# Optimization experiments

Measured on AMD Instinct MI355X. Metric: run time of the kernel, lower is better.

Reference implementation:

```python
import jax, jax.numpy as jnp
import numpy as np

B, IN, H = 4096, 1024, 2048


def setup_inputs() -> dict:
    key = jax.random.key(0)
    ks = jax.random.split(key, 7)
    return {
        "x": jax.random.normal(ks[0], (B, IN), jnp.float32),
        "h": jax.random.normal(ks[1], (B, H), jnp.float32),
        "c": jax.random.normal(ks[2], (B, H), jnp.float32),
        "w_ih": jax.random.normal(ks[3], (4 * H, IN), jnp.float32) * 0.02,
        "w_hh": jax.random.normal(ks[4], (4 * H, H), jnp.float32) * 0.02,
        "b_ih": jax.random.normal(ks[5], (4 * H,), jnp.float32) * 0.02,
        "b_hh": jax.random.normal(ks[6], (4 * H,), jnp.float32) * 0.02,
    }


def reference(x, h, c, w_ih, w_hh, b_ih, b_hh):
    act = jnp.sin  # custom gate activation (Sine_activation repo)
    # Combined GEMMs: same math as the 8 separate F.linear calls.
    # gates: [B, 4H], chunk order along dim 0 of weights: f, i, ic, o
    gates = (x @ w_ih.T + b_ih) + (h @ w_hh.T + b_hh)
    f_in, i_in, ic_in, o_in = jnp.split(gates, 4, axis=-1)
    ft = jax.nn.sigmoid(f_in)
    it = jax.nn.sigmoid(i_in)
    i_cands = act(ic_in)
    ct = c * ft + i_cands * it
    ot = jax.nn.sigmoid(o_in)
    ht = ot * act(ct)
    return (ht, ct)
```

## Files before the change

kernel.cpp:

```cpp
#include <hip/hip_runtime.h>

typedef __attribute__((ext_vector_type(8))) short short8;
typedef __attribute__((ext_vector_type(4))) float f32x4;

#define BDIM 4096
#define INDIM 1024
#define HDIM 2048
#define KDIM 3072
#define NDIM 8192
#define OUT_HALF 8388608
#define NKT 96

__device__ __forceinline__ unsigned short f2bf(float f) {
  unsigned u = __float_as_uint(f);
  u += 0x7FFFu + ((u >> 16) & 1u);
  return (unsigned short)(u >> 16);
}

__device__ __forceinline__ float sigmoidf_(float x) {
  return 1.0f / (1.0f + __expf(-x));
}

__global__ __launch_bounds__(256) void pack_a(const float* __restrict__ x,
                                              const float* __restrict__ hh,
                                              unsigned short* __restrict__ A) {
  int idx = blockIdx.x * 256 + threadIdx.x;
  int m = idx / 384;
  int k0 = (idx - m * 384) * 8;
  const float* src = (k0 < INDIM) ? (x + (size_t)m * INDIM + k0)
                                  : (hh + (size_t)m * HDIM + (k0 - INDIM));
  float4 lo = ((const float4*)src)[0];
  float4 hi = ((const float4*)src)[1];
  union { unsigned short us[8]; uint4 v; } o;
  o.us[0] = f2bf(lo.x); o.us[1] = f2bf(lo.y); o.us[2] = f2bf(lo.z); o.us[3] = f2bf(lo.w);
  o.us[4] = f2bf(hi.x); o.us[5] = f2bf(hi.y); o.us[6] = f2bf(hi.z); o.us[7] = f2bf(hi.w);
  *(uint4*)(A + (size_t)m * KDIM + k0) = o.v;
}

__global__ __launch_bounds__(256) void pack_w(const float* __restrict__ w_ih,
                                              const float* __restrict__ w_hh,
                                              const float* __restrict__ b_ih,
                                              const float* __restrict__ b_hh,
                                              unsigned short* __restrict__ W,
                                              float* __restrict__ bias) {
  int idx = blockIdx.x * 256 + threadIdx.x;
  int np = idx / 384;
  int rem = idx - np * 384;
  int k0 = rem * 8;
  int j = np >> 2;
  int g = np & 3;
  int n = g * HDIM + j;
  const float* src = (k0 < INDIM) ? (w_ih + (size_t)n * INDIM + k0)
                                  : (w_hh + (size_t)n * HDIM + (k0 - INDIM));
  float4 lo = ((const float4*)src)[0];
  float4 hi = ((const float4*)src)[1];
  union { unsigned short us[8]; uint4 v; } o;
  o.us[0] = f2bf(lo.x); o.us[1] = f2bf(lo.y); o.us[2] = f2bf(lo.z); o.us[3] = f2bf(lo.w);
  o.us[4] = f2bf(hi.x); o.us[5] = f2bf(hi.y); o.us[6] = f2bf(hi.z); o.us[7] = f2bf(hi.w);
  *(uint4*)(W + (size_t)np * KDIM + k0) = o.v;
  if (rem == 0) bias[np] = b_ih[n] + b_hh[n];
}

__device__ __forceinline__ void gload_lds16(const void* g, void* l) {
  __builtin_amdgcn_global_load_lds(
      (const __attribute__((address_space(1))) void*)g,
      (__attribute__((address_space(3))) void*)l, 16, 0, 0);
}

__global__ __launch_bounds__(512, 2) void lstm_gemm(
    const unsigned short* __restrict__ A,
    const unsigned short* __restrict__ W,
    const float* __restrict__ bias,
    const float* __restrict__ c,
    float* __restrict__ out) {
  extern __shared__ char smem[];

  const int tid = threadIdx.x;
  const int lane = tid & 63;
  const int wid = tid >> 6;

  const int bid = blockIdx.x;
  const int local = bid >> 3;
  const int tm = (bid & 7) * 2 + (local & 1);
  const int tn = local >> 1;

  int rowA0, clA0, rowA1, clA1, rowB0, clB0, rowB1, clB1;
  {
    int P0 = wid * 1024 + lane * 16;
    int P1 = 8192 + wid * 1024 + lane * 16;
    int r2, cp, cg;
    r2 = P0 >> 7; cp = (P0 >> 4) & 7; cg = cp ^ (r2 & 7);
    rowA0 = r2 * 2 + (cg >> 2); clA0 = cg & 3;
    r2 = P1 >> 7; cp = (P1 >> 4) & 7; cg = cp ^ (r2 & 7);
    rowA1 = r2 * 2 + (cg >> 2); clA1 = cg & 3;
    rowB0 = rowA0; clB0 = clA0;
    rowB1 = rowA1; clB1 = clA1;
  }
  const unsigned short* srcA0 = A + (size_t)(tm * 256 + rowA0) * KDIM + clA0 * 8;
  const unsigned short* srcA1 = A + (size_t)(tm * 256 + rowA1) * KDIM + clA1 * 8;
  const unsigned short* srcB0 = W + (size_t)(tn * 256 + rowB0) * KDIM + clB0 * 8;
  const unsigned short* srcB1 = W + (size_t)(tn * 256 + rowB1) * KDIM + clB1 * 8;
  const int ldA0 = wid * 1024;
  const int ldA1 = 8192 + wid * 1024;
  const int ldB0 = 16384 + wid * 1024;
  const int ldB1 = 24576 + wid * 1024;

  const int fr = lane & 15;
  const int fq = lane >> 4;
  const int wr = wid >> 2;
  const int wc = wid & 3;
  const int frh = fr >> 1;
  const int clA = (((fr & 1) << 2) | fq) ^ frh;
  const int aconst = wr * 8192 + frh * 128 + clA * 16;
  const int bconst = 16384 + wc * 4096 + frh * 128 + clA * 16;

  f32x4 acc[8][4] = {};

#pragma unroll
  for (int tt = 0; tt < 3; ++tt) {
    char* lb = smem + tt * 32768;
    gload_lds16(srcA0 + tt * 32, lb + ldA0);
    gload_lds16(srcA1 + tt * 32, lb + ldA1);
    gload_lds16(srcB0 + tt * 32, lb + ldB0);
    gload_lds16(srcB1 + tt * 32, lb + ldB1);
  }

#define TILE_BODY(T, VMSTR, STAGE_)                                          \
  do {                                                                       \
    const char* rb = smem + ((T) & 3) * 32768;                               \
    char* lb = smem + (((T) + 3) & 3) * 32768;                               \
    if (STAGE_) {                                                            \
      gload_lds16(srcA0 + (size_t)((T) + 3) * 32, lb + ldA0);                \
      gload_lds16(srcA1 + (size_t)((T) + 3) * 32, lb + ldA1);                \
    }                                                                        \
    asm volatile("s_waitcnt vmcnt(" VMSTR ")" ::: "memory");                 \
    __builtin_amdgcn_s_barrier();                                            \
    short8 bf_[4], af[4];                                                    \
    _Pragma("unroll")                                                        \
    for (int ni = 0; ni < 4; ++ni)                                           \
      bf_[ni] = *(const short8*)(rb + bconst + ni * 1024);                   \
    _Pragma("unroll")                                                        \
    for (int mi = 0; mi < 4; ++mi)                                           \
      af[mi] = *(const short8*)(rb + aconst + mi * 1024);                    \
    __builtin_amdgcn_s_setprio(1);                                           \
    _Pragma("unroll")                                                        \
    for (int mi = 0; mi < 4; ++mi)                                           \
      _Pragma("unroll")                                                      \
      for (int ni = 0; ni < 4; ++ni)                                         \
        acc[mi][ni] = __builtin_amdgcn_mfma_f32_16x16x32_bf16(               \
            af[mi], bf_[ni], acc[mi][ni], 0, 0, 0);                          \
    __builtin_amdgcn_s_setprio(0);                                           \
    if (STAGE_) {                                                            \
      gload_lds16(srcB0 + (size_t)((T) + 3) * 32, lb + ldB0);                \
      gload_lds16(srcB1 + (size_t)((T) + 3) * 32, lb + ldB1);                \
    }                                                                        \
    short8 ag[4];                                                            \
    _Pragma("unroll")                                                        \
    for (int mi = 0; mi < 4; ++mi)                                           \
      ag[mi] = *(const short8*)(rb + aconst + (mi + 4) * 1024);              \
    __builtin_amdgcn_s_setprio(1);                                           \
    _Pragma("unroll")                                                        \
    for (int mi = 0; mi < 4; ++mi)                                           \
      _Pragma("unroll")                                                      \
      for (int ni = 0; ni < 4; ++ni)                                         \
        acc[mi + 4][ni] = __builtin_amdgcn_mfma_f32_16x16x32_bf16(           \
            ag[mi], bf_[ni], acc[mi + 4][ni], 0, 0, 0);                      \
    __builtin_amdgcn_s_setprio(0);                                           \
    asm volatile("s_waitcnt lgkmcnt(0)" ::: "memory");                       \
    __builtin_amdgcn_s_barrier();                                            \
  } while (0)

  for (int t = 0; t < NKT - 3; ++t) TILE_BODY(t, "10", true);
  TILE_BODY(NKT - 3, "8", false);
  TILE_BODY(NKT - 2, "4", false);
  TILE_BODY(NKT - 1, "0", false);
#undef TILE_BODY

  const int jw = fr;
  const int jg = tn * 64 + wc * 16 + jw;
  const f32x4 bi = *(const f32x4*)(bias + tn * 256 + wc * 64 + jw * 4);
  float* ep = (float*)smem + wid * 1024;

#pragma unroll
  for (int mi = 0; mi < 8; ++mi) {
#pragma unroll
    for (int ni = 0; ni < 4; ++ni)
#pragma unroll
      for (int r = 0; r < 4; ++r)
        ep[(fq * 4 + r) * 64 + ni * 16 + fr] = acc[mi][ni][r];
    asm volatile("s_waitcnt lgkmcnt(0)" ::: "memory");
#pragma unroll
    for (int t4 = 0; t4 < 4; ++t4) {
      const int row = fq + t4 * 4;
      f32x4 g4 = *(const f32x4*)(ep + row * 64 + jw * 4);
      const float f_in = g4[0] + bi[0];
      const float i_in = g4[1] + bi[1];
      const float ic_in = g4[2] + bi[2];
      const float o_in = g4[3] + bi[3];
      const float ft = sigmoidf_(f_in);
      const float it = sigmoidf_(i_in);
      const float ics = __sinf(ic_in);
      const int mg = tm * 256 + wr * 128 + mi * 16 + row;
      const float cv = c[(size_t)mg * HDIM + jg];
      const float ct = cv * ft + ics * it;
      const float ot = sigmoidf_(o_in);
      const float ht = ot * __sinf(ct);
      out[(size_t)mg * HDIM + jg] = ht;
      out[OUT_HALF + (size_t)mg * HDIM + jg] = ct;
    }
    asm volatile("s_waitcnt lgkmcnt(0)" ::: "memory");
  }
}

extern "C" void kernel_launch(void* const* d_in, const int* in_sizes, int n_in,
                              void* d_out, int out_size, void* d_ws, size_t ws_size,
                              hipStream_t stream) {
  const float* x    = (const float*)d_in[0];
  const float* h    = (const float*)d_in[1];
  const float* c    = (const float*)d_in[2];
  const float* w_ih = (const float*)d_in[3];
  const float* w_hh = (const float*)d_in[4];
  const float* b_ih = (const float*)d_in[5];
  const float* b_hh = (const float*)d_in[6];
  float* out = (float*)d_out;

  char* ws = (char*)d_ws;
  unsigned short* Abf = (unsigned short*)ws;
  unsigned short* Wbf = (unsigned short*)(ws + 25165824);
  float* bias = (float*)(ws + 25165824 + 50331648);

  static_assert(sizeof(void*) == 8, "");
  hipFuncSetAttribute((const void*)lstm_gemm,
                      hipFuncAttributeMaxDynamicSharedMemorySize, 131072);

  pack_a<<<6144, 256, 0, stream>>>(x, h, Abf);
  pack_w<<<12288, 256, 0, stream>>>(w_ih, w_hh, b_ih, b_hh, Wbf, bias);
  lstm_gemm<<<512, 512, 131072, stream>>>(Abf, Wbf, bias, c, out);
}
```

Baseline: 233.5 us.

## Prefetch next K-tile LDS fragments into registers and merge barriers per tile

Restructures the GEMM main loop so the A and B fragments for the next K tile are read from LDS into registers while the current tile's second MFMA half runs. The two barriers per iteration become one, placed mid-tile, and sched_barrier fences pin the instruction order. The vmcnt wait thresholds are recomputed to match. This hides LDS read latency behind MFMAs at the cost of more live registers and a tighter synchronization scheme that could race if the counts are wrong.

```diff
diff --git a/kernel.cpp b/kernel.cpp
--- a/kernel.cpp
+++ b/kernel.cpp
@@ -67,6 +67,8 @@
       (__attribute__((address_space(3))) void*)l, 16, 0, 0);
 }
 
+#define SB0 __builtin_amdgcn_sched_barrier(0)
+
 __global__ __launch_bounds__(512, 2) void lstm_gemm(
     const unsigned short* __restrict__ A,
     const unsigned short* __restrict__ W,
@@ -84,7 +86,7 @@
   const int tm = (bid & 7) * 2 + (local & 1);
   const int tn = local >> 1;
 
-  int rowA0, clA0, rowA1, clA1, rowB0, clB0, rowB1, clB1;
+  int rowA0, clA0, rowA1, clA1;
   {
     int P0 = wid * 1024 + lane * 16;
     int P1 = 8192 + wid * 1024 + lane * 16;
@@ -93,13 +95,11 @@
     rowA0 = r2 * 2 + (cg >> 2); clA0 = cg & 3;
     r2 = P1 >> 7; cp = (P1 >> 4) & 7; cg = cp ^ (r2 & 7);
     rowA1 = r2 * 2 + (cg >> 2); clA1 = cg & 3;
-    rowB0 = rowA0; clB0 = clA0;
-    rowB1 = rowA1; clB1 = clA1;
   }
   const unsigned short* srcA0 = A + (size_t)(tm * 256 + rowA0) * KDIM + clA0 * 8;
   const unsigned short* srcA1 = A + (size_t)(tm * 256 + rowA1) * KDIM + clA1 * 8;
-  const unsigned short* srcB0 = W + (size_t)(tn * 256 + rowB0) * KDIM + clB0 * 8;
-  const unsigned short* srcB1 = W + (size_t)(tn * 256 + rowB1) * KDIM + clB1 * 8;
+  const unsigned short* srcB0 = W + (size_t)(tn * 256 + rowA0) * KDIM + clA0 * 8;
+  const unsigned short* srcB1 = W + (size_t)(tn * 256 + rowA1) * KDIM + clA1 * 8;
   const int ldA0 = wid * 1024;
   const int ldA1 = 8192 + wid * 1024;
   const int ldB0 = 16384 + wid * 1024;
@@ -115,6 +115,7 @@
   const int bconst = 16384 + wc * 4096 + frh * 128 + clA * 16;
 
   f32x4 acc[8][4] = {};
+  short8 af[4], bf_[4], ag[4];
 
 #pragma unroll
   for (int tt = 0; tt < 3; ++tt) {
@@ -124,24 +125,28 @@
     gload_lds16(srcB0 + tt * 32, lb + ldB0);
     gload_lds16(srcB1 + tt * 32, lb + ldB1);
   }
-
-#define TILE_BODY(T, VMSTR, STAGE_)                                          \
+  asm volatile("s_waitcnt vmcnt(8)" ::: "memory");
+  __builtin_amdgcn_s_barrier(); SB0;
+#pragma unroll
+  for (int mi = 0; mi < 4; ++mi)
+    af[mi] = *(const short8*)(smem + aconst + mi * 1024);
+#pragma unroll
+  for (int ni = 0; ni < 4; ++ni)
+    bf_[ni] = *(const short8*)(smem + bconst + ni * 1024);
+
+#define TILE_BODY(T, VMSTR, STAGE_, PREF_)                                   \
   do {                                                                       \
     const char* rb = smem + ((T) & 3) * 32768;                               \
+    const char* rbn = smem + (((T) + 1) & 3) * 32768;                        \
     char* lb = smem + (((T) + 3) & 3) * 32768;                               \
     if (STAGE_) {                                                            \
       gload_lds16(srcA0 + (size_t)((T) + 3) * 32, lb + ldA0);                \
       gload_lds16(srcA1 + (size_t)((T) + 3) * 32, lb + ldA1);                \
     }                                                                        \
-    asm volatile("s_waitcnt vmcnt(" VMSTR ")" ::: "memory");                 \
-    __builtin_amdgcn_s_barrier();                                            \
-    short8 bf_[4], af[4];                                                    \
-    _Pragma("unroll")                                                        \
-    for (int ni = 0; ni < 4; ++ni)                                           \
-      bf_[ni] = *(const short8*)(rb + bconst + ni * 1024);                   \
     _Pragma("unroll")                                                        \
     for (int mi = 0; mi < 4; ++mi)                                           \
-      af[mi] = *(const short8*)(rb + aconst + mi * 1024);                    \
+      ag[mi] = *(const short8*)(rb + aconst + (mi + 4) * 1024);              \
+    SB0;                                                                     \
     __builtin_amdgcn_s_setprio(1);                                           \
     _Pragma("unroll")                                                        \
     for (int mi = 0; mi < 4; ++mi)                                           \
@@ -154,10 +159,15 @@
       gload_lds16(srcB0 + (size_t)((T) + 3) * 32, lb + ldB0);                \
       gload_lds16(srcB1 + (size_t)((T) + 3) * 32, lb + ldB1);                \
     }                                                                        \
-    short8 ag[4];                                                            \
-    _Pragma("unroll")                                                        \
-    for (int mi = 0; mi < 4; ++mi)                                           \
-      ag[mi] = *(const short8*)(rb + aconst + (mi + 4) * 1024);              \
+    asm volatile("s_waitcnt vmcnt(" VMSTR ")" ::: "memory");                 \
+    asm volatile("s_waitcnt lgkmcnt(0)" ::: "memory");                       \
+    __builtin_amdgcn_s_barrier(); SB0;                                       \
+    if (PREF_) {                                                             \
+      _Pragma("unroll")                                                      \
+      for (int mi = 0; mi < 4; ++mi)                                         \
+        af[mi] = *(const short8*)(rbn + aconst + mi * 1024);                 \
+    }                                                                        \
+    SB0;                                                                     \
     __builtin_amdgcn_s_setprio(1);                                           \
     _Pragma("unroll")                                                        \
     for (int mi = 0; mi < 4; ++mi)                                           \
@@ -166,14 +176,17 @@
         acc[mi + 4][ni] = __builtin_amdgcn_mfma_f32_16x16x32_bf16(           \
             ag[mi], bf_[ni], acc[mi + 4][ni], 0, 0, 0);                      \
     __builtin_amdgcn_s_setprio(0);                                           \
-    asm volatile("s_waitcnt lgkmcnt(0)" ::: "memory");                       \
-    __builtin_amdgcn_s_barrier();                                            \
+    if (PREF_) {                                                             \
+      _Pragma("unroll")                                                      \
+      for (int ni = 0; ni < 4; ++ni)                                         \
+        bf_[ni] = *(const short8*)(rbn + bconst + ni * 1024);                \
+    }                                                                        \
   } while (0)
 
-  for (int t = 0; t < NKT - 3; ++t) TILE_BODY(t, "10", true);
-  TILE_BODY(NKT - 3, "8", false);
-  TILE_BODY(NKT - 2, "4", false);
-  TILE_BODY(NKT - 1, "0", false);
+  for (int t = 0; t < NKT - 3; ++t) TILE_BODY(t, "8", true, true);
+  TILE_BODY(NKT - 3, "4", false, true);
+  TILE_BODY(NKT - 2, "0", false, true);
+  TILE_BODY(NKT - 1, "0", false, false);
 #undef TILE_BODY
 
   const int jw = fr;
@@ -229,7 +242,6 @@
   unsigned short* Wbf = (unsigned short*)(ws + 25165824);
   float* bias = (float*)(ws + 25165824 + 50331648);
 
-  static_assert(sizeof(void*) == 8, "");
   hipFuncSetAttribute((const void*)lstm_gemm,
                       hipFuncAttributeMaxDynamicSharedMemorySize, 131072);
 
```

Measured after the change: 222.6 us. -4.6%, faster.

## Restructure GEMM main loop to K=64 double-buffered tiles with split staging

Applied to the files above, without the earlier changes.

The main GEMM loop moves from a 4-deep ring of K=32 tiles to two 64KB buffers of K=64 tiles, and uses a new XOR swizzle. Each tile is split into four MFMA clusters, with A and B halves staged asynchronously between clusters behind barriers, so global-to-LDS loads overlap compute with fewer full-tile syncs. The two pack kernels are merged into one launch, and the epilogue LDS row stride is padded to 68 to reduce bank conflicts. The cost is more barriers per tile and shallower prefetch depth, which may expose memory latency.

```diff
diff --git a/kernel.cpp b/kernel.cpp
--- a/kernel.cpp
+++ b/kernel.cpp
@@ -9,7 +9,8 @@
 #define KDIM 3072
 #define NDIM 8192
 #define OUT_HALF 8388608
-#define NKT 96
+#define NKT 48
+#define ACHUNKS 1572864
 
 __device__ __forceinline__ unsigned short f2bf(float f) {
   unsigned u = __float_as_uint(f);
@@ -21,44 +22,42 @@
   return 1.0f / (1.0f + __expf(-x));
 }
 
-__global__ __launch_bounds__(256) void pack_a(const float* __restrict__ x,
-                                              const float* __restrict__ hh,
-                                              unsigned short* __restrict__ A) {
+__global__ __launch_bounds__(256) void pack_all(
+    const float* __restrict__ x, const float* __restrict__ hh,
+    const float* __restrict__ w_ih, const float* __restrict__ w_hh,
+    const float* __restrict__ b_ih, const float* __restrict__ b_hh,
+    unsigned short* __restrict__ A, unsigned short* __restrict__ W,
+    float* __restrict__ bias) {
   int idx = blockIdx.x * 256 + threadIdx.x;
-  int m = idx / 384;
-  int k0 = (idx - m * 384) * 8;
-  const float* src = (k0 < INDIM) ? (x + (size_t)m * INDIM + k0)
-                                  : (hh + (size_t)m * HDIM + (k0 - INDIM));
-  float4 lo = ((const float4*)src)[0];
-  float4 hi = ((const float4*)src)[1];
-  union { unsigned short us[8]; uint4 v; } o;
-  o.us[0] = f2bf(lo.x); o.us[1] = f2bf(lo.y); o.us[2] = f2bf(lo.z); o.us[3] = f2bf(lo.w);
-  o.us[4] = f2bf(hi.x); o.us[5] = f2bf(hi.y); o.us[6] = f2bf(hi.z); o.us[7] = f2bf(hi.w);
-  *(uint4*)(A + (size_t)m * KDIM + k0) = o.v;
-}
-
-__global__ __launch_bounds__(256) void pack_w(const float* __restrict__ w_ih,
-                                              const float* __restrict__ w_hh,
-                                              const float* __restrict__ b_ih,
-                                              const float* __restrict__ b_hh,
-                                              unsigned short* __restrict__ W,
-                                              float* __restrict__ bias) {
-  int idx = blockIdx.x * 256 + threadIdx.x;
-  int np = idx / 384;
-  int rem = idx - np * 384;
-  int k0 = rem * 8;
-  int j = np >> 2;
-  int g = np & 3;
-  int n = g * HDIM + j;
-  const float* src = (k0 < INDIM) ? (w_ih + (size_t)n * INDIM + k0)
-                                  : (w_hh + (size_t)n * HDIM + (k0 - INDIM));
-  float4 lo = ((const float4*)src)[0];
-  float4 hi = ((const float4*)src)[1];
-  union { unsigned short us[8]; uint4 v; } o;
-  o.us[0] = f2bf(lo.x); o.us[1] = f2bf(lo.y); o.us[2] = f2bf(lo.z); o.us[3] = f2bf(lo.w);
-  o.us[4] = f2bf(hi.x); o.us[5] = f2bf(hi.y); o.us[6] = f2bf(hi.z); o.us[7] = f2bf(hi.w);
-  *(uint4*)(W + (size_t)np * KDIM + k0) = o.v;
-  if (rem == 0) bias[np] = b_ih[n] + b_hh[n];
+  if (idx < ACHUNKS) {
+    int m = idx / 384;
+    int k0 = (idx - m * 384) * 8;
+    const float* src = (k0 < INDIM) ? (x + (size_t)m * INDIM + k0)
+                                    : (hh + (size_t)m * HDIM + (k0 - INDIM));
+    float4 lo = ((const float4*)src)[0];
+    float4 hi = ((const float4*)src)[1];
+    union { unsigned short us[8]; uint4 v; } o;
+    o.us[0] = f2bf(lo.x); o.us[1] = f2bf(lo.y); o.us[2] = f2bf(lo.z); o.us[3] = f2bf(lo.w);
+    o.us[4] = f2bf(hi.x); o.us[5] = f2bf(hi.y); o.us[6] = f2bf(hi.z); o.us[7] = f2bf(hi.w);
+    *(uint4*)(A + (size_t)m * KDIM + k0) = o.v;
+  } else {
+    idx -= ACHUNKS;
+    int np = idx / 384;
+    int rem = idx - np * 384;
+    int k0 = rem * 8;
+    int j = np >> 2;
+    int g = np & 3;
+    int n = g * HDIM + j;
+    const float* src = (k0 < INDIM) ? (w_ih + (size_t)n * INDIM + k0)
+                                    : (w_hh + (size_t)n * HDIM + (k0 - INDIM));
+    float4 lo = ((const float4*)src)[0];
+    float4 hi = ((const float4*)src)[1];
+    union { unsigned short us[8]; uint4 v; } o;
+    o.us[0] = f2bf(lo.x); o.us[1] = f2bf(lo.y); o.us[2] = f2bf(lo.z); o.us[3] = f2bf(lo.w);
+    o.us[4] = f2bf(hi.x); o.us[5] = f2bf(hi.y); o.us[6] = f2bf(hi.z); o.us[7] = f2bf(hi.w);
+    *(uint4*)(W + (size_t)np * KDIM + k0) = o.v;
+    if (rem == 0) bias[np] = b_ih[n] + b_hh[n];
+  }
 }
 
 __device__ __forceinline__ void gload_lds16(const void* g, void* l) {
@@ -84,102 +83,127 @@
   const int tm = (bid & 7) * 2 + (local & 1);
   const int tn = local >> 1;
 
-  int rowA0, clA0, rowA1, clA1, rowB0, clB0, rowB1, clB1;
-  {
-    int P0 = wid * 1024 + lane * 16;
-    int P1 = 8192 + wid * 1024 + lane * 16;
-    int r2, cp, cg;
-    r2 = P0 >> 7; cp = (P0 >> 4) & 7; cg = cp ^ (r2 & 7);
-    rowA0 = r2 * 2 + (cg >> 2); clA0 = cg & 3;
-    r2 = P1 >> 7; cp = (P1 >> 4) & 7; cg = cp ^ (r2 & 7);
-    rowA1 = r2 * 2 + (cg >> 2); clA1 = cg & 3;
-    rowB0 = rowA0; clB0 = clA0;
-    rowB1 = rowA1; clB1 = clA1;
-  }
-  const unsigned short* srcA0 = A + (size_t)(tm * 256 + rowA0) * KDIM + clA0 * 8;
-  const unsigned short* srcA1 = A + (size_t)(tm * 256 + rowA1) * KDIM + clA1 * 8;
-  const unsigned short* srcB0 = W + (size_t)(tn * 256 + rowB0) * KDIM + clB0 * 8;
-  const unsigned short* srcB1 = W + (size_t)(tn * 256 + rowB1) * KDIM + clB1 * 8;
-  const int ldA0 = wid * 1024;
-  const int ldA1 = 8192 + wid * 1024;
-  const int ldB0 = 16384 + wid * 1024;
-  const int ldB1 = 24576 + wid * 1024;
+  const int clog = (tid & 7) ^ ((tid >> 3) & 7);
+  const int srow = tid >> 3;
+  const unsigned short* pA00 = A + (size_t)(tm * 256 +   0 + srow) * KDIM + clog * 8;
+  const unsigned short* pA01 = A + (size_t)(tm * 256 +  64 + srow) * KDIM + clog * 8;
+  const unsigned short* pA10 = A + (size_t)(tm * 256 + 128 + srow) * KDIM + clog * 8;
+  const unsigned short* pA11 = A + (size_t)(tm * 256 + 192 + srow) * KDIM + clog * 8;
+  const unsigned short* pB00 = W + (size_t)(tn * 256 +   0 + srow) * KDIM + clog * 8;
+  const unsigned short* pB01 = W + (size_t)(tn * 256 +  64 + srow) * KDIM + clog * 8;
+  const unsigned short* pB10 = W + (size_t)(tn * 256 + 128 + srow) * KDIM + clog * 8;
+  const unsigned short* pB11 = W + (size_t)(tn * 256 + 192 + srow) * KDIM + clog * 8;
+  const int dwid = wid * 1024;
 
   const int fr = lane & 15;
   const int fq = lane >> 4;
   const int wr = wid >> 2;
   const int wc = wid & 3;
-  const int frh = fr >> 1;
-  const int clA = (((fr & 1) << 2) | fq) ^ frh;
-  const int aconst = wr * 8192 + frh * 128 + clA * 16;
-  const int bconst = 16384 + wc * 4096 + frh * 128 + clA * 16;
+  int colK[2];
+#pragma unroll
+  for (int ks = 0; ks < 2; ++ks) colK[ks] = (((ks * 4 + fq) ^ (fr & 7)) << 4);
+  const int abase = wr * 16384 + fr * 128;
+  const int bbase = 32768 + wc * 8192 + fr * 128;
 
   f32x4 acc[8][4] = {};
-
-#pragma unroll
-  for (int tt = 0; tt < 3; ++tt) {
-    char* lb = smem + tt * 32768;
-    gload_lds16(srcA0 + tt * 32, lb + ldA0);
-    gload_lds16(srcA1 + tt * 32, lb + ldA1);
-    gload_lds16(srcB0 + tt * 32, lb + ldB0);
-    gload_lds16(srcB1 + tt * 32, lb + ldB1);
-  }
-
-#define TILE_BODY(T, VMSTR, STAGE_)                                          \
-  do {                                                                       \
-    const char* rb = smem + ((T) & 3) * 32768;                               \
-    char* lb = smem + (((T) + 3) & 3) * 32768;                               \
-    if (STAGE_) {                                                            \
-      gload_lds16(srcA0 + (size_t)((T) + 3) * 32, lb + ldA0);                \
-      gload_lds16(srcA1 + (size_t)((T) + 3) * 32, lb + ldA1);                \
-    }                                                                        \
-    asm volatile("s_waitcnt vmcnt(" VMSTR ")" ::: "memory");                 \
-    __builtin_amdgcn_s_barrier();                                            \
-    short8 bf_[4], af[4];                                                    \
+  short8 fa[4][2], fb0[2][2], fb1[2][2];
+
+  char* cb = smem;
+  char* nb = smem + 65536;
+
+#define BAR __builtin_amdgcn_s_barrier()
+#define LGKM0 asm volatile("s_waitcnt lgkmcnt(0)" ::: "memory")
+#define STG_A(DB, T1)                                                        \
+  do {                                                                       \
+    gload_lds16(pA00 + (size_t)(T1) * 64, (DB) + 0 + dwid);                  \
+    gload_lds16(pA01 + (size_t)(T1) * 64, (DB) + 8192 + dwid);               \
+    gload_lds16(pA10 + (size_t)(T1) * 64, (DB) + 16384 + dwid);              \
+    gload_lds16(pA11 + (size_t)(T1) * 64, (DB) + 24576 + dwid);              \
+  } while (0)
+#define STG_B_H0(DB, T2)                                                     \
+  do {                                                                       \
+    gload_lds16(pB00 + (size_t)(T2) * 64, (DB) + 32768 + dwid);              \
+    gload_lds16(pB01 + (size_t)(T2) * 64, (DB) + 40960 + dwid);              \
+  } while (0)
+#define STG_B_H1(DB, T2)                                                     \
+  do {                                                                       \
+    gload_lds16(pB10 + (size_t)(T2) * 64, (DB) + 49152 + dwid);              \
+    gload_lds16(pB11 + (size_t)(T2) * 64, (DB) + 57344 + dwid);              \
+  } while (0)
+#define READ_FA(MIH)                                                         \
+  _Pragma("unroll")                                                          \
+  for (int mi = 0; mi < 4; ++mi)                                             \
     _Pragma("unroll")                                                        \
-    for (int ni = 0; ni < 4; ++ni)                                           \
-      bf_[ni] = *(const short8*)(rb + bconst + ni * 1024);                   \
+    for (int ks = 0; ks < 2; ++ks)                                           \
+      fa[mi][ks] = *(const short8*)(cb + abase + ((MIH)*4 + mi) * 2048 + colK[ks]);
+#define READ_FB(DST, NIH)                                                    \
+  _Pragma("unroll")                                                          \
+  for (int ni = 0; ni < 2; ++ni)                                             \
     _Pragma("unroll")                                                        \
-    for (int mi = 0; mi < 4; ++mi)                                           \
-      af[mi] = *(const short8*)(rb + aconst + mi * 1024);                    \
+    for (int ks = 0; ks < 2; ++ks)                                           \
+      DST[ni][ks] = *(const short8*)(cb + bbase + ((NIH)*2 + ni) * 2048 + colK[ks]);
+#define CLUST(FB, MIH, NIH)                                                  \
+  do {                                                                       \
     __builtin_amdgcn_s_setprio(1);                                           \
     _Pragma("unroll")                                                        \
-    for (int mi = 0; mi < 4; ++mi)                                           \
+    for (int ks = 0; ks < 2; ++ks)                                           \
       _Pragma("unroll")                                                      \
-      for (int ni = 0; ni < 4; ++ni)                                         \
-        acc[mi][ni] = __builtin_amdgcn_mfma_f32_16x16x32_bf16(               \
-            af[mi], bf_[ni], acc[mi][ni], 0, 0, 0);                          \
+      for (int mi = 0; mi < 4; ++mi)                                         \
+        _Pragma("unroll")                                                    \
+        for (int ni = 0; ni < 2; ++ni)                                       \
+          acc[(MIH)*4 + mi][(NIH)*2 + ni] =                                  \
+              __builtin_amdgcn_mfma_f32_16x16x32_bf16(                       \
+                  fa[mi][ks], FB[ni][ks], acc[(MIH)*4 + mi][(NIH)*2 + ni],   \
+                  0, 0, 0);                                                  \
     __builtin_amdgcn_s_setprio(0);                                           \
-    if (STAGE_) {                                                            \
-      gload_lds16(srcB0 + (size_t)((T) + 3) * 32, lb + ldB0);                \
-      gload_lds16(srcB1 + (size_t)((T) + 3) * 32, lb + ldB1);                \
-    }                                                                        \
-    short8 ag[4];                                                            \
-    _Pragma("unroll")                                                        \
-    for (int mi = 0; mi < 4; ++mi)                                           \
-      ag[mi] = *(const short8*)(rb + aconst + (mi + 4) * 1024);              \
-    __builtin_amdgcn_s_setprio(1);                                           \
-    _Pragma("unroll")                                                        \
-    for (int mi = 0; mi < 4; ++mi)                                           \
-      _Pragma("unroll")                                                      \
-      for (int ni = 0; ni < 4; ++ni)                                         \
-        acc[mi + 4][ni] = __builtin_amdgcn_mfma_f32_16x16x32_bf16(           \
-            ag[mi], bf_[ni], acc[mi + 4][ni], 0, 0, 0);                      \
-    __builtin_amdgcn_s_setprio(0);                                           \
-    asm volatile("s_waitcnt lgkmcnt(0)" ::: "memory");                       \
-    __builtin_amdgcn_s_barrier();                                            \
-  } while (0)
-
-  for (int t = 0; t < NKT - 3; ++t) TILE_BODY(t, "10", true);
-  TILE_BODY(NKT - 3, "8", false);
-  TILE_BODY(NKT - 2, "4", false);
-  TILE_BODY(NKT - 1, "0", false);
-#undef TILE_BODY
+  } while (0)
+
+#define TILE(T, SA_, SB_, VMSTR)                                             \
+  do {                                                                       \
+                                                                     \
+    READ_FA(0);                                                              \
+    READ_FB(fb0, 0);                                                         \
+    if (SA_) STG_A(nb, (T) + 1);                                             \
+    BAR; LGKM0; CLUST(fb0, 0, 0); BAR;                                       \
+                                                                     \
+    READ_FB(fb1, 1);                                                         \
+    BAR; LGKM0; CLUST(fb1, 0, 1); BAR;                                       \
+                                                                     \
+    READ_FA(1);                                                              \
+    if (SB_) STG_B_H0(cb, (T) + 2);                                          \
+    BAR; LGKM0; CLUST(fb0, 1, 0); BAR;                                       \
+                                                                     \
+    if (SB_) STG_B_H1(cb, (T) + 2);                                          \
+    asm volatile("s_waitcnt vmcnt(" VMSTR ")" ::: "memory");                 \
+    BAR; CLUST(fb1, 1, 1); BAR;                                              \
+  } while (0)
+
+  STG_A(cb, 0);
+  STG_B_H0(cb, 0); STG_B_H1(cb, 0);
+  STG_B_H0(nb, 1); STG_B_H1(nb, 1);
+  asm volatile("s_waitcnt vmcnt(4)" ::: "memory");
+  BAR;
+
+  for (int t = 0; t <= 45; ++t) {
+    TILE(t, true, true, "4");
+    char* tmp = cb; cb = nb; nb = tmp;
+  }
+  TILE(46, true, false, "0");
+  { char* tmp = cb; cb = nb; nb = tmp; }
+  TILE(47, false, false, "0");
+
+#undef TILE
+#undef CLUST
+#undef READ_FB
+#undef READ_FA
+#undef STG_B_H1
+#undef STG_B_H0
+#undef STG_A
 
   const int jw = fr;
   const int jg = tn * 64 + wc * 16 + jw;
   const f32x4 bi = *(const f32x4*)(bias + tn * 256 + wc * 64 + jw * 4);
-  float* ep = (float*)smem + wid * 1024;
+  float* ep = (float*)smem + wid * 1152;
 
 #pragma unroll
   for (int mi = 0; mi < 8; ++mi) {
@@ -187,12 +211,12 @@
     for (int ni = 0; ni < 4; ++ni)
 #pragma unroll
       for (int r = 0; r < 4; ++r)
-        ep[(fq * 4 + r) * 64 + ni * 16 + fr] = acc[mi][ni][r];
-    asm volatile("s_waitcnt lgkmcnt(0)" ::: "memory");
+        ep[(fq * 4 + r) * 68 + ni * 16 + fr] = acc[mi][ni][r];
+    LGKM0;
 #pragma unroll
     for (int t4 = 0; t4 < 4; ++t4) {
       const int row = fq + t4 * 4;
-      f32x4 g4 = *(const f32x4*)(ep + row * 64 + jw * 4);
+      f32x4 g4 = *(const f32x4*)(ep + row * 68 + jw * 4);
       const float f_in = g4[0] + bi[0];
       const float i_in = g4[1] + bi[1];
       const float ic_in = g4[2] + bi[2];
@@ -208,8 +232,10 @@
       out[(size_t)mg * HDIM + jg] = ht;
       out[OUT_HALF + (size_t)mg * HDIM + jg] = ct;
     }
-    asm volatile("s_waitcnt lgkmcnt(0)" ::: "memory");
+    LGKM0;
   }
+#undef LGKM0
+#undef BAR
 }
 
 extern "C" void kernel_launch(void* const* d_in, const int* in_sizes, int n_in,
@@ -229,11 +255,9 @@
   unsigned short* Wbf = (unsigned short*)(ws + 25165824);
   float* bias = (float*)(ws + 25165824 + 50331648);
 
-  static_assert(sizeof(void*) == 8, "");
   hipFuncSetAttribute((const void*)lstm_gemm,
                       hipFuncAttributeMaxDynamicSharedMemorySize, 131072);
 
-  pack_a<<<6144, 256, 0, stream>>>(x, h, Abf);
-  pack_w<<<12288, 256, 0, stream>>>(w_ih, w_hh, b_ih, b_hh, Wbf, bias);
+  pack_all<<<18432, 256, 0, stream>>>(x, h, w_ih, w_hh, b_ih, b_hh, Abf, Wbf, bias);
   lstm_gemm<<<512, 512, 131072, stream>>>(Abf, Wbf, bias, c, out);
 }
```

Result: faster. 221.4 us (-5.2%).
